# Optimization experiments

Measured on AMD Instinct MI355X. Metric: run time of the kernel, lower is better.

## Reference

```python
import jax, jax.numpy as jnp
import numpy as np

N = 131072          # number of depos
W = 10              # static raster window (cells per dim); covers 2*nsigma*sigma_max/spacing
NSIGMA = 3.0
SQRT2 = 1.4142135623730951


def setup_inputs() -> dict:
    key = jax.random.key(0)
    k1, k2, k3, k4 = jax.random.split(key, 4)
    # Gaussian widths in [0.25, 0.75] (distance units) so +-3 sigma fits in W=10 cells of 0.5
    sigma = 0.25 + 0.5 * jax.random.uniform(k1, (N, 3), dtype=jnp.float32)
    time = 100.0 * jax.random.uniform(k2, (N,), dtype=jnp.float32)
    charge = 5000.0 * jax.random.uniform(k3, (N,), dtype=jnp.float32)
    tail = 50.0 * jax.random.normal(k4, (N, 3), dtype=jnp.float32)
    grid_spacing = jnp.array([0.5, 0.5, 0.5], dtype=jnp.float32)
    return {"sigma": sigma, "time": time, "charge": charge, "tail": tail,
            "grid_spacing": grid_spacing}


def reference(sigma, time, charge, tail, grid_spacing):
    # _transform with pdims=(1,2), tdim=-1: point = [tail[:,1], tail[:,2], time]
    pt = jnp.stack([tail[:, 1], tail[:, 2], time], axis=-1)          # [N,3]
    g = grid_spacing                                                  # [3]
    # window start grid index per depo per dim (nsigma cutoff)
    imin = jnp.floor((pt - NSIGMA * sigma) / g)                       # [N,3]
    # cell edge coordinates for W cells -> W+1 edges
    k = jnp.arange(W + 1, dtype=pt.dtype)                             # [W+1]
    edges = (imin[:, :, None] + k[None, None, :]) * g[None, :, None]  # [N,3,W+1]
    # integrated Gaussian per cell per dim via erf differences
    z = (edges - pt[:, :, None]) / (sigma[:, :, None] * SQRT2)
    cdf = 0.5 * (1.0 + jax.lax.erf(z))
    w = cdf[..., 1:] - cdf[..., :-1]                                  # [N,3,W]
    # separable outer product scaled by charge -> [N,W,W,W]
    rasters = (charge[:, None, None, None]
               * w[:, 0, :, None, None]
               * w[:, 1, None, :, None]
               * w[:, 2, None, None, :])
    offsets = imin.astype(jnp.int32)                                  # [N,3]
    return rasters, offsets
```

## Files before the change

### kernel.cpp

```cpp
#include <hip/hip_runtime.h>
#include <math.h>

#define WCELLS 10
#define WAVES_PER_BLOCK 4
#define BLOCK 256

typedef float f32x4 __attribute__((ext_vector_type(4)));

__global__ __launch_bounds__(BLOCK) void raster_kernel(
    const float* __restrict__ sigma,
    const float* __restrict__ time_,
    const float* __restrict__ charge,
    const float* __restrict__ tail,
    const float* __restrict__ gsp,
    float* __restrict__ out_r,
    float* __restrict__ out_off,
    int n, int niter)
{
    __shared__ float s_w01[WAVES_PER_BLOCK][2][12];
    __shared__ float s_w2 [WAVES_PER_BLOCK][12];
    __shared__ float s_qw01[WAVES_PER_BLOCK][100];

    const int wave = threadIdx.x >> 6;
    const int lane = threadIdx.x & 63;
    const int nwaves = gridDim.x * WAVES_PER_BLOCK;
    int d = blockIdx.x * WAVES_PER_BLOCK + wave;

    const float g0 = gsp[0], g1 = gsp[1], g2 = gsp[2];

    for (int it = 0; it < niter; ++it, d += nwaves) {
        const bool active = (d < n);

        const int dim = lane / 11;
        const int k   = lane - dim * 11;
        float cdf = 0.0f, iminf = 0.0f;
        if (active && lane < 33) {
            float pt = (dim == 0) ? tail[(size_t)d*3 + 1]
                     : (dim == 1) ? tail[(size_t)d*3 + 2]
                     : time_[d];
            float sg = sigma[(size_t)d*3 + dim];
            float g  = (dim == 0) ? g0 : (dim == 1) ? g1 : g2;
            iminf = floorf((pt - 3.0f * sg) / g);
            float edge = (iminf + (float)k) * g;
            float z = (edge - pt) / (sg * 1.4142135623730951f);
            cdf = 0.5f * (1.0f + erff(z));
        }
        float cdf1 = __shfl_down(cdf, 1);
        if (active && lane < 33) {
            if (k < 10) {
                float wv = cdf1 - cdf;
                if (dim < 2) s_w01[wave][dim][k] = wv;
                else         s_w2 [wave][k]      = wv;
            }
            if (k == 0) {
                out_off[(size_t)d*3 + dim] = iminf;
            }
        }
        __syncthreads();

        if (active) {
            float q = charge[d];
            int i = lane;
            s_qw01[wave][i] = q * s_w01[wave][0][i/10] * s_w01[wave][1][i%10];
            int i2 = lane + 64;
            if (i2 < 100)
                s_qw01[wave][i2] = q * s_w01[wave][0][i2/10] * s_w01[wave][1][i2%10];
        }
        __syncthreads();

        if (active) {
            float* base = out_r + (size_t)d * 1000;
            const float* qw = s_qw01[wave];
            const float* w2 = s_w2[wave];
            #pragma unroll
            for (int cc = 0; cc < 4; ++cc) {
                int c = lane + cc * 64;
                if (c < 250) {
                    int f = 4 * c;
                    f32x4 v;
                    v.x = qw[(f    ) / 10] * w2[(f    ) % 10];
                    v.y = qw[(f + 1) / 10] * w2[(f + 1) % 10];
                    v.z = qw[(f + 2) / 10] * w2[(f + 2) % 10];
                    v.w = qw[(f + 3) / 10] * w2[(f + 3) % 10];
                    *reinterpret_cast<f32x4*>(base + f) = v;
                }
            }
        }
        __syncthreads();
    }
}

extern "C" void kernel_launch(void* const* d_in, const int* in_sizes, int n_in,
                              void* d_out, int out_size, void* d_ws, size_t ws_size,
                              hipStream_t stream) {
    const float* sigma  = (const float*)d_in[0];
    const float* time_  = (const float*)d_in[1];
    const float* charge = (const float*)d_in[2];
    const float* tail   = (const float*)d_in[3];
    const float* gsp    = (const float*)d_in[4];

    const int n = in_sizes[1];
    float* out_r   = (float*)d_out;
    float* out_off = out_r + (size_t)n * (WCELLS * WCELLS * WCELLS);

    const int blocks = 4096;
    const int nwaves = blocks * WAVES_PER_BLOCK;
    const int niter  = (n + nwaves - 1) / nwaves;

    raster_kernel<<<blocks, BLOCK, 0, stream>>>(sigma, time_, charge, tail, gsp,
                                                out_r, out_off, n, niter);
}
```

Before: 110.2 us.

## Drop block barriers, use wave shuffles, and prefetch next depo inputs

Measured after the change: 113.8 us. +3.3%, slower.

```diff
diff --git a/kernel.cpp b/kernel.cpp
--- a/kernel.cpp
+++ b/kernel.cpp
@@ -1,7 +1,6 @@
 #include <hip/hip_runtime.h>
 #include <math.h>
 
-#define WCELLS 10
 #define WAVES_PER_BLOCK 4
 #define BLOCK 256
 
@@ -17,9 +16,8 @@
     float* __restrict__ out_off,
     int n, int niter)
 {
-    __shared__ float s_w01[WAVES_PER_BLOCK][2][12];
+    __shared__ float s_qw01[WAVES_PER_BLOCK][104];
     __shared__ float s_w2 [WAVES_PER_BLOCK][12];
-    __shared__ float s_qw01[WAVES_PER_BLOCK][100];
 
     const int wave = threadIdx.x >> 6;
     const int lane = threadIdx.x & 63;
@@ -28,45 +26,63 @@
 
     const float g0 = gsp[0], g1 = gsp[1], g2 = gsp[2];
 
-    for (int it = 0; it < niter; ++it, d += nwaves) {
+    const int dim = lane / 11;
+    const int k   = lane - dim * 11;
+    const float gdim = (dim == 0) ? g0 : (dim == 1) ? g1 : g2;
+
+    const int i0a = lane;
+    const int s0a = i0a / 10, s1a = 11 + i0a % 10;
+    const int i0b = lane + 64;
+    const int s0b = i0b / 10, s1b = 11 + i0b % 10;
+
+    float pt = 0.f, sg = 1.f, q = 0.f;
+    if (d < n) {
+        if (lane < 33) {
+            pt = (dim == 0) ? tail[(size_t)d*3 + 1]
+               : (dim == 1) ? tail[(size_t)d*3 + 2]
+               : time_[d];
+            sg = sigma[(size_t)d*3 + dim];
+        }
+        q = charge[d];
+    }
+
+    for (int it = 0; it < niter; ++it) {
         const bool active = (d < n);
+        const int dn = d + nwaves;
 
-        const int dim = lane / 11;
-        const int k   = lane - dim * 11;
         float cdf = 0.0f, iminf = 0.0f;
-        if (active && lane < 33) {
-            float pt = (dim == 0) ? tail[(size_t)d*3 + 1]
-                     : (dim == 1) ? tail[(size_t)d*3 + 2]
-                     : time_[d];
-            float sg = sigma[(size_t)d*3 + dim];
-            float g  = (dim == 0) ? g0 : (dim == 1) ? g1 : g2;
-            iminf = floorf((pt - 3.0f * sg) / g);
-            float edge = (iminf + (float)k) * g;
+        if (lane < 33) {
+            iminf = floorf((pt - 3.0f * sg) / gdim);
+            float edge = (iminf + (float)k) * gdim;
             float z = (edge - pt) / (sg * 1.4142135623730951f);
             cdf = 0.5f * (1.0f + erff(z));
         }
         float cdf1 = __shfl_down(cdf, 1);
-        if (active && lane < 33) {
-            if (k < 10) {
-                float wv = cdf1 - cdf;
-                if (dim < 2) s_w01[wave][dim][k] = wv;
-                else         s_w2 [wave][k]      = wv;
+        float wv = cdf1 - cdf;
+
+        if (active && lane < 33 && k == 0)
+            out_off[(size_t)d*3 + dim] = iminf;
+
+        float npt = 0.f, nsg = 1.f, nq = 0.f;
+        if (dn < n) {
+            if (lane < 33) {
+                npt = (dim == 0) ? tail[(size_t)dn*3 + 1]
+                    : (dim == 1) ? tail[(size_t)dn*3 + 2]
+                    : time_[dn];
+                nsg = sigma[(size_t)dn*3 + dim];
             }
-            if (k == 0) {
-                out_off[(size_t)d*3 + dim] = iminf;
-            }
+            nq = charge[dn];
         }
-        __syncthreads();
 
-        if (active) {
-            float q = charge[d];
-            int i = lane;
-            s_qw01[wave][i] = q * s_w01[wave][0][i/10] * s_w01[wave][1][i%10];
-            int i2 = lane + 64;
-            if (i2 < 100)
-                s_qw01[wave][i2] = q * s_w01[wave][0][i2/10] * s_w01[wave][1][i2%10];
+        {
+            float w0a = __shfl(wv, s0a);
+            float w1a = __shfl(wv, s1a);
+            s_qw01[wave][i0a] = q * w0a * w1a;
+            float w0b = __shfl(wv, s0b);
+            float w1b = __shfl(wv, s1b);
+            if (i0b < 100) s_qw01[wave][i0b] = q * w0b * w1b;
+            if (lane >= 22 && lane < 32) s_w2[wave][lane - 22] = wv;
         }
-        __syncthreads();
 
         if (active) {
             float* base = out_r + (size_t)d * 1000;
@@ -86,7 +102,8 @@
                 }
             }
         }
-        __syncthreads();
+
+        d = dn; pt = npt; sg = nsg; q = nq;
     }
 }
 
@@ -101,7 +118,7 @@
 
     const int n = in_sizes[1];
     float* out_r   = (float*)d_out;
-    float* out_off = out_r + (size_t)n * (WCELLS * WCELLS * WCELLS);
+    float* out_off = out_r + (size_t)n * 1000;
 
     const int blocks = 4096;
     const int nwaves = blocks * WAVES_PER_BLOCK;
```
